# Optimization experiments

Measured on AMD Instinct MI355X. Metric: run time of the kernel, lower is better.

## Reference

```python
import jax, jax.numpy as jnp
import numpy as np

N = 30000      # nodes
IN = 768       # input feature dim
C = 128        # hidden channels (= conv out_dim, = gate dim)
HEADS = 4      # attention heads (TransformerConv and Semantic)
DH = 128       # per-head dim (concat=False -> out_channels)
R = 3          # num relations
E = 80000      # edges per relation
NEG = 0.01     # LeakyReLU slope


def setup_inputs() -> dict:
    key = jax.random.key(0)
    ks = iter(jax.random.split(key, 64))
    def nx(shape):
        return jax.random.normal(next(ks), shape, dtype=jnp.float32) * 0.02
    inp = {}
    inp["x"] = jax.random.normal(next(ks), (N, IN), dtype=jnp.float32)
    inp["edges"] = jax.random.randint(next(ks), (R, 2, E), 0, N, dtype=jnp.int32)
    inp["lin1_W"] = nx((IN, C)); inp["lin1_b"] = jnp.zeros((C,), jnp.float32)
    for l in ("l1", "l2"):
        inp[f"{l}_Wq"] = nx((R, C, HEADS * DH)); inp[f"{l}_bq"] = jnp.zeros((R, HEADS * DH), jnp.float32)
        inp[f"{l}_Wk"] = nx((R, C, HEADS * DH)); inp[f"{l}_bk"] = jnp.zeros((R, HEADS * DH), jnp.float32)
        inp[f"{l}_Wv"] = nx((R, C, HEADS * DH)); inp[f"{l}_bv"] = jnp.zeros((R, HEADS * DH), jnp.float32)
        inp[f"{l}_Ws"] = nx((R, C, DH));         inp[f"{l}_bs"] = jnp.zeros((R, DH), jnp.float32)
        inp[f"{l}_gW"] = nx((C + DH, C));        inp[f"{l}_gb"] = jnp.zeros((C,), jnp.float32)
        inp[f"{l}_sW1"] = nx((HEADS, C, C));     inp[f"{l}_sb1"] = jnp.zeros((HEADS, C), jnp.float32)
        inp[f"{l}_sw2"] = nx((HEADS, C))
    inp["lin2_W"] = nx((C, C)); inp["lin2_b"] = jnp.zeros((C,), jnp.float32)
    inp["clf_W"] = nx((C, 2)); inp["clf_b"] = jnp.zeros((2,), jnp.float32)
    return inp


def lrelu(x):
    return jnp.where(x >= 0, x, NEG * x)


def transformer_conv(x, src, dst, Wq, bq, Wk, bk, Wv, bv, Ws, bs):
    # PyG TransformerConv, heads=HEADS, concat=False (head mean), root_weight=True, eval (no dropout)
    n = x.shape[0]
    q = (x @ Wq + bq).reshape(n, HEADS, DH)
    k = (x @ Wk + bk).reshape(n, HEADS, DH)
    v = (x @ Wv + bv).reshape(n, HEADS, DH)
    logits = (q[dst] * k[src]).sum(-1) / np.sqrt(DH)      # [E, H]
    m = jax.ops.segment_max(logits, dst, num_segments=n)  # scatter-softmax (stable)
    a = jnp.exp(logits - m[dst])
    s = jax.ops.segment_sum(a, dst, num_segments=n)
    alpha = a / s[dst]
    agg = jax.ops.segment_sum(alpha[:, :, None] * v[src], dst, num_segments=n)  # [N, H, DH]
    return agg.mean(axis=1) + x @ Ws + bs


def semantic(Hm, sW1, sb1, sw2):
    # Hm: [N, R, C]; per-head scoring MLP -> softmax over relations -> weighted sum, averaged over heads
    t = jnp.tanh(jnp.einsum('nrc,hco->hnro', Hm, sW1) + sb1[:, None, None, :])  # [H, N, R, C]
    scores = jnp.einsum('hnro,ho->hnr', t, sw2).mean(axis=1)                    # [H, R]
    beta = jax.nn.softmax(scores, axis=-1)
    return jnp.einsum('hr,nrc->nc', beta, Hm) / HEADS


def rgt_layer(x, edges, Wq, bq, Wk, bk, Wv, bv, Ws, bs, gW, gb, sW1, sb1, sw2):
    Hs = []
    for r in range(R):  # small fixed relation loop
        src, dst = edges[r, 0], edges[r, 1]
        U = transformer_conv(x, src, dst, Wq[r], bq[r], Wk[r], bk[r], Wv[r], bv[r], Ws[r], bs[r])
        Z = jax.nn.sigmoid(jnp.concatenate([U, x], axis=1) @ gW + gb)
        Hs.append(jnp.tanh(U) * Z + x * (1.0 - Z))
    Hm = jnp.stack(Hs, axis=1)  # [N, R, C]
    return semantic(Hm, sW1, sb1, sw2)


def reference(x, edges, lin1_W, lin1_b,
              l1_Wq, l1_bq, l1_Wk, l1_bk, l1_Wv, l1_bv, l1_Ws, l1_bs, l1_gW, l1_gb, l1_sW1, l1_sb1, l1_sw2,
              l2_Wq, l2_bq, l2_Wk, l2_bk, l2_Wv, l2_bv, l2_Ws, l2_bs, l2_gW, l2_gb, l2_sW1, l2_sb1, l2_sw2,
              lin2_W, lin2_b, clf_W, clf_b):
    h = lrelu(x @ lin1_W + lin1_b)
    h = rgt_layer(h, edges, l1_Wq, l1_bq, l1_Wk, l1_bk, l1_Wv, l1_bv, l1_Ws, l1_bs, l1_gW, l1_gb, l1_sW1, l1_sb1, l1_sw2)
    h = rgt_layer(h, edges, l2_Wq, l2_bq, l2_Wk, l2_bk, l2_Wv, l2_bv, l2_Ws, l2_bs, l2_gW, l2_gb, l2_sW1, l2_sb1, l2_sw2)
    h = lrelu(h @ lin2_W + lin2_b)
    return h @ clf_W + clf_b
```

## Files before the change

kernel.cpp:

```cpp
#include <hip/hip_runtime.h>
#include <math.h>

#define Nn 30000
#define RR 3
#define EE 80000
#define MT_M 235

#define SAP 72
#define EP_LD 68
#define KBIG 0x40000000

typedef __attribute__((ext_vector_type(8))) short bf16x8;
typedef __attribute__((ext_vector_type(4))) float f32x4;

__device__ __forceinline__ unsigned short f2bf(float f) {
    union { float f; unsigned u; } v; v.f = f;
    unsigned r = v.u + 0x7fff + ((v.u >> 16) & 1);
    return (unsigned short)(r >> 16);
}
__device__ __forceinline__ float bf2f(short h) {
    union { unsigned u; float f; } v;
    v.u = ((unsigned)(unsigned short)h) << 16;
    return v.f;
}
__device__ __forceinline__ float fast_tanh(float x) {
    float e = __expf(2.f * x);
    return 1.f - 2.f / (e + 1.f);
}
__device__ __forceinline__ void unpack8(uint4 u, float* f) {
    union { unsigned u; float f; } a;
    a.u = u.x << 16;          f[0] = a.f;
    a.u = u.x & 0xffff0000u;  f[1] = a.f;
    a.u = u.y << 16;          f[2] = a.f;
    a.u = u.y & 0xffff0000u;  f[3] = a.f;
    a.u = u.z << 16;          f[4] = a.f;
    a.u = u.z & 0xffff0000u;  f[5] = a.f;
    a.u = u.w << 16;          f[6] = a.f;
    a.u = u.w & 0xffff0000u;  f[7] = a.f;
}

__device__ __forceinline__ void mfma_core(
    const short* __restrict__ A, int lda,
    const short* __restrict__ A2, int lda2, int ksplit,
    const short* __restrict__ Bt,
    int M, int K, int m0, int n0,
    short* As, short* Bs, f32x4 (&acc)[4][4])
{
    const int t = threadIdx.x;
    const int srow = t >> 3;
    const int scol = (t & 7) << 3;
    const int lane = t & 63;
    const int wave = t >> 6;
    const int wm = (wave >> 1) << 6;
    const int wn = (wave & 1) << 6;
    const int fr = lane & 15;
    const int quad = lane >> 4;

    for (int k0 = 0; k0 < K; k0 += 64) {
        const short* Abase; int kk0, ldax;
        if (k0 < ksplit) { Abase = A;  kk0 = k0;          ldax = lda;  }
        else             { Abase = A2; kk0 = k0 - ksplit; ldax = lda2; }
        #pragma unroll
        for (int rr = 0; rr < 4; rr++) {
            int r = srow + rr * 32;
            int gr = m0 + r;
            bf16x8 va = {0, 0, 0, 0, 0, 0, 0, 0};
            if (gr < M) va = *(const bf16x8*)(Abase + (size_t)gr * ldax + kk0 + scol);
            *(bf16x8*)(As + r * SAP + scol) = va;
        }
        #pragma unroll
        for (int rr = 0; rr < 4; rr++) {
            int r = srow + rr * 32;
            bf16x8 vb = *(const bf16x8*)(Bt + (size_t)(n0 + r) * K + k0 + scol);
            *(bf16x8*)(Bs + r * SAP + scol) = vb;
        }
        __syncthreads();
        #pragma unroll
        for (int kc = 0; kc < 2; kc++) {
            bf16x8 af[4], bfr[4];
            #pragma unroll
            for (int i = 0; i < 4; i++)
                af[i] = *(const bf16x8*)(As + (wm + i * 16 + fr) * SAP + kc * 32 + quad * 8);
            #pragma unroll
            for (int i = 0; i < 4; i++)
                bfr[i] = *(const bf16x8*)(Bs + (wn + i * 16 + fr) * SAP + kc * 32 + quad * 8);
            #pragma unroll
            for (int mi = 0; mi < 4; mi++)
                #pragma unroll
                for (int ni = 0; ni < 4; ni++)
                    acc[mi][ni] = __builtin_amdgcn_mfma_f32_16x16x32_bf16(
                        af[mi], bfr[ni], acc[mi][ni], 0, 0, 0);
        }
        __syncthreads();
    }
}

__global__ __launch_bounds__(256) void gemm_mfma(
    const short* __restrict__ A, int lda,
    const short* __restrict__ A2, int lda2, int ksplit,
    const short* __restrict__ Bt, const float* __restrict__ bias,
    float* __restrict__ C, int ldc, short* __restrict__ Cbf, int ldcbf,
    int M, int K, int act)
{
    __shared__ short As[128 * SAP];
    __shared__ short Bs[128 * SAP];
    f32x4 acc[4][4];
    #pragma unroll
    for (int i = 0; i < 4; i++)
        #pragma unroll
        for (int j = 0; j < 4; j++) acc[i][j] = (f32x4){0.f, 0.f, 0.f, 0.f};
    int m0 = blockIdx.y * 128, n0 = blockIdx.x * 128;
    mfma_core(A, lda, A2, lda2, ksplit, Bt, M, K, m0, n0, As, Bs, acc);

    const int t = threadIdx.x;
    const int lane = t & 63, wave = t >> 6;
    const int wm = (wave >> 1) << 6, wn = (wave & 1) << 6;
    const int fr = lane & 15, quad = lane >> 4;
    float* ws = (float*)As + wave * 16 * EP_LD;
    const int rrow = lane >> 2;
    const int cseg = (lane & 3) << 4;
    #pragma unroll
    for (int mi = 0; mi < 4; mi++) {
        #pragma unroll
        for (int ni = 0; ni < 4; ni++)
            #pragma unroll
            for (int reg = 0; reg < 4; reg++)
                ws[(quad * 4 + reg) * EP_LD + ni * 16 + fr] = acc[mi][ni][reg];
        int gr = m0 + wm + mi * 16 + rrow;
        if (gr >= M) continue;
        int gc = n0 + wn + cseg;
        float vals[16];
        #pragma unroll
        for (int j = 0; j < 16; j++) {
            float v = ws[rrow * EP_LD + cseg + j] + bias[gc + j];
            if (act == 1) v = (v >= 0.f) ? v : 0.01f * v;
            vals[j] = v;
        }
        if (C) {
            float* cp = C + (size_t)gr * ldc + gc;
            #pragma unroll
            for (int j4 = 0; j4 < 4; j4++)
                *(float4*)(cp + j4 * 4) = make_float4(vals[j4 * 4], vals[j4 * 4 + 1],
                                                      vals[j4 * 4 + 2], vals[j4 * 4 + 3]);
        }
        if (Cbf) {
            unsigned pk[8];
            #pragma unroll
            for (int j2 = 0; j2 < 8; j2++)
                pk[j2] = ((unsigned)f2bf(vals[2 * j2 + 1]) << 16) | (unsigned)f2bf(vals[2 * j2]);
            unsigned* bp = (unsigned*)(Cbf + (size_t)gr * ldcbf + gc);
            *(uint4*)bp       = make_uint4(pk[0], pk[1], pk[2], pk[3]);
            *(uint4*)(bp + 4) = make_uint4(pk[4], pk[5], pk[6], pk[7]);
        }
    }
}

__global__ __launch_bounds__(256) void gemm_qkvs(
    const short* __restrict__ A,
    const short* __restrict__ Wt, const float* __restrict__ bias,
    short* __restrict__ qkv3, short* __restrict__ Ubf, int M)
{
    __shared__ short As[128 * SAP];
    __shared__ short Bs[128 * SAP];
    f32x4 acc[4][4];
    #pragma unroll
    for (int i = 0; i < 4; i++)
        #pragma unroll
        for (int j = 0; j < 4; j++) acc[i][j] = (f32x4){0.f, 0.f, 0.f, 0.f};
    int m0 = blockIdx.y * 128, bx = blockIdx.x, n0 = bx * 128;
    mfma_core(A, 128, A, 128, KBIG, Wt, M, 128, m0, n0, As, Bs, acc);

    const int t = threadIdx.x;
    const int lane = t & 63, wave = t >> 6;
    const int wm = (wave >> 1) << 6, wn = (wave & 1) << 6;
    const int fr = lane & 15, quad = lane >> 4;
    float* ws = (float*)As + wave * 16 * EP_LD;
    const int rrow = lane >> 2;
    const int cseg = (lane & 3) << 4;
    #pragma unroll
    for (int mi = 0; mi < 4; mi++) {
        #pragma unroll
        for (int ni = 0; ni < 4; ni++)
            #pragma unroll
            for (int reg = 0; reg < 4; reg++)
                ws[(quad * 4 + reg) * EP_LD + ni * 16 + fr] = acc[mi][ni][reg];
        int gr = m0 + wm + mi * 16 + rrow;
        if (gr >= M) continue;
        int lc = wn + cseg;
        float vals[16];
        #pragma unroll
        for (int j = 0; j < 16; j++)
            vals[j] = ws[rrow * EP_LD + cseg + j] + bias[n0 + lc + j];
        unsigned pk[8];
        #pragma unroll
        for (int j2 = 0; j2 < 8; j2++)
            pk[j2] = ((unsigned)f2bf(vals[2 * j2 + 1]) << 16) | (unsigned)f2bf(vals[2 * j2]);
        short* dst;
        if (bx < 36) {
            int r = bx / 12;
            dst = qkv3 + ((size_t)(r * Nn + gr)) * 1536 + (bx - r * 12) * 128 + lc;
        } else {
            dst = Ubf + (size_t)gr * 384 + (bx - 36) * 128 + lc;
        }
        unsigned* bp = (unsigned*)dst;
        *(uint4*)bp       = make_uint4(pk[0], pk[1], pk[2], pk[3]);
        *(uint4*)(bp + 4) = make_uint4(pk[4], pk[5], pk[6], pk[7]);
    }
}

__global__ __launch_bounds__(256) void gate_mfma(
    const short* __restrict__ Ubf,
    const short* __restrict__ Hbf,
    const short* __restrict__ gWt, const float* __restrict__ gb,
    const float* __restrict__ Hf,
    float* __restrict__ Hm, short* __restrict__ HmBf,
    int M)
{
    __shared__ short As[128 * SAP];
    __shared__ short Bs[128 * SAP];
    f32x4 acc[4][4];
    #pragma unroll
    for (int i = 0; i < 4; i++)
        #pragma unroll
        for (int j = 0; j < 4; j++) acc[i][j] = (f32x4){0.f, 0.f, 0.f, 0.f};
    int r = blockIdx.z;
    int m0 = blockIdx.y * 128;
    mfma_core(Ubf + r * 128, 384, Hbf, 128, 128, gWt, M, 256, m0, 0, As, Bs, acc);

    const int t = threadIdx.x;
    const int lane = t & 63, wave = t >> 6;
    const int wm = (wave >> 1) << 6, wn = (wave & 1) << 6;
    const int fr = lane & 15, quad = lane >> 4;
    float* ws = (float*)As + wave * 16 * EP_LD;
    const int rrow = lane >> 2;
    const int cseg = (lane & 3) << 4;
    #pragma unroll
    for (int mi = 0; mi < 4; mi++) {
        #pragma unroll
        for (int ni = 0; ni < 4; ni++)
            #pragma unroll
            for (int reg = 0; reg < 4; reg++)
                ws[(quad * 4 + reg) * EP_LD + ni * 16 + fr] = acc[mi][ni][reg];
        int gr = m0 + wm + mi * 16 + rrow;
        if (gr >= M) continue;
        int gc = wn + cseg;
        const short* up = Ubf + (size_t)gr * 384 + r * 128 + gc;
        const float* hp = Hf + (size_t)gr * 128 + gc;
        float uv[16], hv[16];
        uint4 u0 = *(const uint4*)up;
        uint4 u1 = *(const uint4*)(up + 8);
        unpack8(u0, uv); unpack8(u1, uv + 8);
        #pragma unroll
        for (int j4 = 0; j4 < 4; j4++)
            *(float4*)(hv + j4 * 4) = *(const float4*)(hp + j4 * 4);
        float vals[16];
        #pragma unroll
        for (int j = 0; j < 16; j++) {
            float g = ws[rrow * EP_LD + cseg + j] + gb[gc + j];
            float z = 1.f / (1.f + __expf(-g));
            vals[j] = fast_tanh(uv[j]) * z + hv[j] * (1.f - z);
        }
        float* cp = Hm + (size_t)gr * 384 + r * 128 + gc;
        #pragma unroll
        for (int j4 = 0; j4 < 4; j4++)
            *(float4*)(cp + j4 * 4) = make_float4(vals[j4 * 4], vals[j4 * 4 + 1],
                                                  vals[j4 * 4 + 2], vals[j4 * 4 + 3]);
        unsigned pk[8];
        #pragma unroll
        for (int j2 = 0; j2 < 8; j2++)
            pk[j2] = ((unsigned)f2bf(vals[2 * j2 + 1]) << 16) | (unsigned)f2bf(vals[2 * j2]);
        unsigned* bp = (unsigned*)(HmBf + (size_t)gr * 384 + r * 128 + gc);
        *(uint4*)bp       = make_uint4(pk[0], pk[1], pk[2], pk[3]);
        *(uint4*)(bp + 4) = make_uint4(pk[4], pk[5], pk[6], pk[7]);
    }
}

__global__ __launch_bounds__(256) void semantic_mfma(
    const short* __restrict__ HmBf, const short* __restrict__ sW1t,
    const float* __restrict__ sb1, const float* __restrict__ sw2,
    float* __restrict__ partial, int M)
{
    __shared__ short As[128 * SAP];
    __shared__ short Bs[128 * SAP];
    __shared__ float red4[4];
    f32x4 acc[4][4];
    #pragma unroll
    for (int i = 0; i < 4; i++)
        #pragma unroll
        for (int j = 0; j < 4; j++) acc[i][j] = (f32x4){0.f, 0.f, 0.f, 0.f};
    int head = blockIdx.x, r = blockIdx.z;
    int m0 = blockIdx.y * 128, n0 = head * 128;
    mfma_core(HmBf + r * 128, 384, HmBf + r * 128, 384, KBIG, sW1t, M, 128, m0, n0, As, Bs, acc);
    const int t = threadIdx.x;
    const int lane = t & 63, wave = t >> 6;
    const int wm = (wave >> 1) << 6, wn = (wave & 1) << 6;
    const int fr = lane & 15, quad = lane >> 4;
    float local = 0.f;
    #pragma unroll
    for (int ni = 0; ni < 4; ni++) {
        int gc = n0 + wn + ni * 16 + fr;
        float b = sb1[gc], w2 = sw2[gc];
        #pragma unroll
        for (int mi = 0; mi < 4; mi++) {
            #pragma unroll
            for (int reg = 0; reg < 4; reg++) {
                int gr = m0 + wm + mi * 16 + quad * 4 + reg;
                if (gr >= M) continue;
                local += fast_tanh(acc[mi][ni][reg] + b) * w2;
            }
        }
    }
    #pragma unroll
    for (int off = 1; off < 64; off <<= 1) local += __shfl_xor(local, off);
    if (lane == 0) red4[wave] = local;
    __syncthreads();
    if (t == 0)
        partial[(head * 3 + r) * MT_M + blockIdx.y] = red4[0] + red4[1] + red4[2] + red4[3];
}

__global__ void reduce12_kernel(const float* __restrict__ partial, float* __restrict__ scores)
{
    int z = blockIdx.x;
    int lane = threadIdx.x;
    float s = 0.f;
    for (int i = lane; i < MT_M; i += 64) s += partial[z * MT_M + i];
    #pragma unroll
    for (int off = 1; off < 64; off <<= 1) s += __shfl_xor(s, off);
    if (lane == 0) scores[z] = s;
}

__global__ void compute_w_kernel(const float* __restrict__ scores, float* __restrict__ w, float invN)
{
    if (blockIdx.x == 0 && threadIdx.x == 0) {
        float wr[3] = {0.f, 0.f, 0.f};
        for (int h = 0; h < 4; h++) {
            float s0 = scores[h * 3 + 0] * invN;
            float s1 = scores[h * 3 + 1] * invN;
            float s2 = scores[h * 3 + 2] * invN;
            float mx = fmaxf(s0, fmaxf(s1, s2));
            float e0 = __expf(s0 - mx), e1 = __expf(s1 - mx), e2 = __expf(s2 - mx);
            float inv = 1.f / (e0 + e1 + e2);
            wr[0] += 0.25f * e0 * inv;
            wr[1] += 0.25f * e1 * inv;
            wr[2] += 0.25f * e2 * inv;
        }
        w[0] = wr[0]; w[1] = wr[1]; w[2] = wr[2];
    }
}

__global__ void mix_kernel(const float* __restrict__ Hm, const float* __restrict__ w,
                           float* __restrict__ h, short* __restrict__ hbf, int total4)
{
    int i = blockIdx.x * blockDim.x + threadIdx.x;
    if (i >= total4) return;
    int n = i >> 5, c4 = (i & 31) << 2;
    const float* row = Hm + (size_t)n * 384 + c4;
    float4 a = *(const float4*)row;
    float4 b = *(const float4*)(row + 128);
    float4 c = *(const float4*)(row + 256);
    float w0 = w[0], w1 = w[1], w2 = w[2];
    float4 v = make_float4(w0 * a.x + w1 * b.x + w2 * c.x,
                           w0 * a.y + w1 * b.y + w2 * c.y,
                           w0 * a.z + w1 * b.z + w2 * c.z,
                           w0 * a.w + w1 * b.w + w2 * c.w);
    *(float4*)(h + (size_t)n * 128 + c4) = v;
    unsigned p0 = ((unsigned)f2bf(v.y) << 16) | (unsigned)f2bf(v.x);
    unsigned p1 = ((unsigned)f2bf(v.w) << 16) | (unsigned)f2bf(v.z);
    *(uint2*)(hbf + (size_t)n * 128 + c4) = make_uint2(p0, p1);
}

__global__ void convert_bf16_kernel(const float* __restrict__ src, unsigned* __restrict__ dst, int n_pairs)
{
    int i = blockIdx.x * blockDim.x + threadIdx.x;
    if (i >= n_pairs) return;
    float2 f = ((const float2*)src)[i];
    dst[i] = ((unsigned)f2bf(f.y) << 16) | (unsigned)f2bf(f.x);
}

__global__ void prep_global_kernel(const float* __restrict__ lin1_W, const float* __restrict__ lin2_W,
                                   short* __restrict__ lin1Wt, short* __restrict__ lin2Wt)
{
    int id = blockIdx.x * blockDim.x + threadIdx.x;
    if (id < 98304) {
        int n = id / 768, k = id % 768;
        lin1Wt[id] = (short)f2bf(lin1_W[k * 128 + n]);
    } else if (id < 114688) {
        int r = id - 98304;
        int n = r / 128, k = r % 128;
        lin2Wt[r] = (short)f2bf(lin2_W[k * 128 + n]);
    }
}

__global__ void prep_layer_kernel(
    const float* __restrict__ Wq, const float* __restrict__ Wk, const float* __restrict__ Wv,
    const float* __restrict__ Ws, const float* __restrict__ bq, const float* __restrict__ bk,
    const float* __restrict__ bv, const float* __restrict__ bs,
    const float* __restrict__ gW, const float* __restrict__ sW1,
    short* __restrict__ qkvsWt, short* __restrict__ gWt,
    short* __restrict__ sW1t, float* __restrict__ qkvsB)
{
    const int S0 = 638976;
    const int S1 = S0 + 32768;
    const int S2 = S1 + 65536;
    const int S3 = S2 + 4992;
    int id = blockIdx.x * blockDim.x + threadIdx.x;
    if (id < S0) {
        int n = id / 128, k = id - n * 128;
        float v;
        if (n < 4608) {
            int r = n / 1536, j = n - r * 1536;
            if (j < 512)       v = Wq[(size_t)r * 65536 + k * 512 + j];
            else if (j < 1024) v = Wk[(size_t)r * 65536 + k * 512 + (j - 512)];
            else               v = Wv[(size_t)r * 65536 + k * 512 + (j - 1024)];
        } else {
            int m = n - 4608;
            int r = m / 128, c = m - r * 128;
            v = Ws[(size_t)r * 16384 + k * 128 + c];
        }
        qkvsWt[id] = (short)f2bf(v);
    } else if (id < S1) {
        int q = id - S0;
        int n = q / 256, k = q - n * 256;
        gWt[q] = (short)f2bf(gW[k * 128 + n]);
    } else if (id < S2) {
        int q = id - S1;
        int h = q / 16384, rem = q - h * 16384;
        int n = rem / 128, k = rem - n * 128;
        sW1t[q] = (short)f2bf(sW1[(size_t)h * 16384 + k * 128 + n]);
    } else if (id < S3) {
        int q = id - S2;
        float v;
        if (q < 4608) {
            int r = q / 1536, j = q - r * 1536;
            if (j < 512)       v = bq[r * 512 + j];
            else if (j < 1024) v = bk[r * 512 + (j - 512)];
            else               v = bv[r * 512 + (j - 1024)];
        } else {
            v = bs[q - 4608];
        }
        qkvsB[q] = v;
    }
}

__global__ void zero_i32_kernel(int* __restrict__ p, int n)
{
    int i = blockIdx.x * blockDim.x + threadIdx.x;
    if (i < n) p[i] = 0;
}

__global__ void hist3_kernel(const int* __restrict__ edges, int* __restrict__ cnt3)
{
    int i = blockIdx.x * blockDim.x + threadIdx.x;
    if (i >= 3 * EE) return;
    int r = i / EE, e = i - r * EE;
    int d = edges[(size_t)r * 2 * EE + EE + e];
    atomicAdd(&cnt3[r * Nn + d], 1);
}

__global__ __launch_bounds__(1024) void scan3_kernel(const int* __restrict__ cnt3,
                                                     int* __restrict__ rowptr3)
{
    __shared__ int part[1024];
    const int r = blockIdx.x;
    const int* cnt = cnt3 + r * Nn;
    int* rowptr = rowptr3 + r * (Nn + 1);
    int tid = threadIdx.x;
    int per = (Nn + 1023) >> 10;
    int base = tid * per;
    int s = 0;
    for (int i = 0; i < per; i++) {
        int idx = base + i;
        if (idx < Nn) s += cnt[idx];
    }
    part[tid] = s;
    __syncthreads();
    for (int off = 1; off < 1024; off <<= 1) {
        int val = (tid >= off) ? part[tid - off] : 0;
        __syncthreads();
        part[tid] += val;
        __syncthreads();
    }
    int excl = (tid == 0) ? 0 : part[tid - 1];
    for (int i = 0; i < per; i++) {
        int idx = base + i;
        if (idx < Nn) { rowptr[idx] = excl; excl += cnt[idx]; }
    }
    if (tid == 1023) rowptr[Nn] = part[1023];
}

__global__ void scatter3_kernel(const int* __restrict__ edges,
                                const int* __restrict__ rowptr3, int* __restrict__ fill3,
                                int* __restrict__ col3)
{
    int i = blockIdx.x * blockDim.x + threadIdx.x;
    if (i >= 3 * EE) return;
    int r = i / EE, e = i - r * EE;
    int src = edges[(size_t)r * 2 * EE + e];
    int d   = edges[(size_t)r * 2 * EE + EE + e];
    int pos = rowptr3[r * (Nn + 1) + d] + atomicAdd(&fill3[r * Nn + d], 1);
    col3[r * EE + pos] = src;
}

__global__ __launch_bounds__(256) void attn_kernel(
    const short* __restrict__ qkv3,
    const int* __restrict__ rowptr3, const int* __restrict__ col3,
    short* __restrict__ Ubf)
{
    int wid = ((blockIdx.x * blockDim.x + threadIdx.x) >> 6);
    int lane = threadIdx.x & 63;
    if (wid >= 3 * Nn) return;
    int r = wid / Nn, n = wid - r * Nn;
    const short* qkv = qkv3 + (size_t)r * Nn * 1536;
    const int* rowptr = rowptr3 + r * (Nn + 1);
    const int* colb = col3 + r * EE;
    int beg = rowptr[n], end = rowptr[n + 1];

    uint4 qv = ((const uint4*)(qkv + (size_t)n * 1536))[lane];
    float qf[8];
    unpack8(qv, qf);

    float m = -INFINITY, s = 0.f;
    float acc[8] = {0.f, 0.f, 0.f, 0.f, 0.f, 0.f, 0.f, 0.f};
    const float scale = 0.088388347648318447f;

    for (int i = beg; i < end; i++) {
        int src = colb[i];
        const short* base = qkv + (size_t)src * 1536;
        uint4 kv4 = ((const uint4*)(base + 512))[lane];
        uint4 vv4 = ((const uint4*)(base + 1024))[lane];
        float kf[8];
        unpack8(kv4, kf);
        float p = qf[0] * kf[0] + qf[1] * kf[1] + qf[2] * kf[2] + qf[3] * kf[3]
                + qf[4] * kf[4] + qf[5] * kf[5] + qf[6] * kf[6] + qf[7] * kf[7];
        p += __shfl_xor(p, 1);
        p += __shfl_xor(p, 2);
        p += __shfl_xor(p, 4);
        p += __shfl_xor(p, 8);
        float l = p * scale;
        float nm = fmaxf(m, l);
        float sc = __expf(m - nm);
        float pe = __expf(l - nm);
        float vf[8];
        unpack8(vv4, vf);
        s = s * sc + pe;
        #pragma unroll
        for (int j = 0; j < 8; j++) acc[j] = acc[j] * sc + pe * vf[j];
        m = nm;
    }

    float inv = (s > 0.f) ? 1.f / s : 0.f;
    #pragma unroll
    for (int j = 0; j < 8; j++) acc[j] *= inv;
    #pragma unroll
    for (int j = 0; j < 8; j++) acc[j] += __shfl_xor(acc[j], 16);
    #pragma unroll
    for (int j = 0; j < 8; j++) acc[j] += __shfl_xor(acc[j], 32);

    if (lane < 16) {
        short* urow = Ubf + (size_t)n * 384 + r * 128 + lane * 8;
        uint4 old = *(uint4*)urow;
        float sv[8];
        unpack8(old, sv);
        #pragma unroll
        for (int j = 0; j < 8; j++) sv[j] += 0.25f * acc[j];
        unsigned p0 = ((unsigned)f2bf(sv[1]) << 16) | (unsigned)f2bf(sv[0]);
        unsigned p1 = ((unsigned)f2bf(sv[3]) << 16) | (unsigned)f2bf(sv[2]);
        unsigned p2 = ((unsigned)f2bf(sv[5]) << 16) | (unsigned)f2bf(sv[4]);
        unsigned p3 = ((unsigned)f2bf(sv[7]) << 16) | (unsigned)f2bf(sv[6]);
        *(uint4*)urow = make_uint4(p0, p1, p2, p3);
    }
}

__global__ void clf_kernel(const float* __restrict__ t, const float* __restrict__ W,
                           const float* __restrict__ b, float* __restrict__ out, int M)
{
    int n = blockIdx.x * blockDim.x + threadIdx.x;
    if (n >= M) return;
    const float* row = t + (size_t)n * 128;
    float a0 = b[0], a1 = b[1];
    #pragma unroll
    for (int kk = 0; kk < 128; kk++) {
        float a = row[kk];
        a0 += a * W[kk * 2];
        a1 += a * W[kk * 2 + 1];
    }
    out[n * 2] = a0;
    out[n * 2 + 1] = a1;
}

extern "C" void kernel_launch(void* const* d_in, const int* in_sizes, int n_in,
                              void* d_out, int out_size, void* d_ws, size_t ws_size,
                              hipStream_t stream)
{
    const float* x      = (const float*)d_in[0];
    const int*   edges  = (const int*)d_in[1];
    const float* lin1_W = (const float*)d_in[2];
    const float* lin1_b = (const float*)d_in[3];
    const int L0 = 4, L1 = 17;
    const float* lin2_W = (const float*)d_in[30];
    const float* lin2_b = (const float*)d_in[31];
    const float* clf_W  = (const float*)d_in[32];
    const float* clf_b  = (const float*)d_in[33];
    float* out = (float*)d_out;

    char* w = (char*)d_ws;
    size_t off = 0;
    auto alloc = [&](size_t bytes) { void* p = w + off; off = (off + bytes + 255) & ~(size_t)255; return p; };
    float* h      = (float*)alloc((size_t)Nn * 128 * 4);
    short* h_bf   = (short*)alloc((size_t)Nn * 128 * 2);
    short* U_bf   = (short*)alloc((size_t)Nn * 384 * 2);
    char* BIG     = (char*)alloc((size_t)3 * Nn * 1536 * 2);
    short* qkv3   = (short*)BIG;
    short* x_bf   = (short*)BIG;
    float* Hm     = (float*)BIG;
    short* Hm_bf  = (short*)(BIG + (size_t)Nn * 384 * 4);
    float* lin2o  = (float*)BIG;
    short* lin1Wt = (short*)alloc((size_t)98304 * 2);
    short* lin2Wt = (short*)alloc((size_t)16384 * 2);
    short* qkvsWt = (short*)alloc((size_t)2 * 638976 * 2);
    short* gWt    = (short*)alloc((size_t)2 * 32768 * 2);
    short* sW1t   = (short*)alloc((size_t)2 * 65536 * 2);
    float* qkvsB  = (float*)alloc((size_t)2 * 4992 * 4);
    int* rowptr3  = (int*)alloc((size_t)3 * (Nn + 1) * 4);
    int* cnt3     = (int*)alloc((size_t)3 * Nn * 4);
    int* col3     = (int*)alloc((size_t)3 * EE * 4);
    float* partial = (float*)alloc((size_t)12 * MT_M * 4);
    float* scores = (float*)alloc(12 * 4);
    float* wmix   = (float*)alloc(3 * 4);

    const int MT = MT_M;
    dim3 blk(256);

    {
        int n_pairs = Nn * 768 / 2;
        convert_bf16_kernel<<<(n_pairs + 255) / 256, blk, 0, stream>>>(x, (unsigned*)x_bf, n_pairs);
        prep_global_kernel<<<(114688 + 255) / 256, blk, 0, stream>>>(lin1_W, lin2_W, lin1Wt, lin2Wt);
        for (int l = 0; l < 2; l++) {
            int base = (l == 0) ? L0 : L1;
            prep_layer_kernel<<<(742272 + 255) / 256, blk, 0, stream>>>(
                (const float*)d_in[base + 0], (const float*)d_in[base + 2], (const float*)d_in[base + 4],
                (const float*)d_in[base + 6], (const float*)d_in[base + 1], (const float*)d_in[base + 3],
                (const float*)d_in[base + 5], (const float*)d_in[base + 7],
                (const float*)d_in[base + 8], (const float*)d_in[base + 10],
                qkvsWt + (size_t)l * 638976, gWt + (size_t)l * 32768,
                sW1t + (size_t)l * 65536, qkvsB + (size_t)l * 4992);
        }
        zero_i32_kernel<<<(3 * Nn + 255) / 256, blk, 0, stream>>>(cnt3, 3 * Nn);
        hist3_kernel<<<(3 * EE + 255) / 256, blk, 0, stream>>>(edges, cnt3);
        scan3_kernel<<<3, 1024, 0, stream>>>(cnt3, rowptr3);
        zero_i32_kernel<<<(3 * Nn + 255) / 256, blk, 0, stream>>>(cnt3, 3 * Nn);
        scatter3_kernel<<<(3 * EE + 255) / 256, blk, 0, stream>>>(edges, rowptr3, cnt3, col3);
    }

    gemm_mfma<<<dim3(1, MT), blk, 0, stream>>>(
        x_bf, 768, x_bf, 768, KBIG, lin1Wt, lin1_b, h, 128, h_bf, 128, Nn, 768, 1);

    for (int l = 0; l < 2; l++) {
        int base = (l == 0) ? L0 : L1;
        const float* gb  = (const float*)d_in[base + 9];
        const float* sb1 = (const float*)d_in[base + 11];
        const float* sw2 = (const float*)d_in[base + 12];
        short* lqkvsWt = qkvsWt + (size_t)l * 638976;
        short* lgWt    = gWt + (size_t)l * 32768;
        short* lsW1t   = sW1t + (size_t)l * 65536;
        float* lqkvsB  = qkvsB + (size_t)l * 4992;

        gemm_qkvs<<<dim3(39, MT), blk, 0, stream>>>(
            h_bf, lqkvsWt, lqkvsB, qkv3, U_bf, Nn);

        attn_kernel<<<(3 * Nn + 3) / 4, blk, 0, stream>>>(qkv3, rowptr3, col3, U_bf);

        gate_mfma<<<dim3(1, MT, 3), blk, 0, stream>>>(
            U_bf, h_bf, lgWt, gb, h, Hm, Hm_bf, Nn);

        semantic_mfma<<<dim3(4, MT, 3), blk, 0, stream>>>(Hm_bf, lsW1t, sb1, sw2, partial, Nn);
        reduce12_kernel<<<12, 64, 0, stream>>>(partial, scores);
        compute_w_kernel<<<1, 64, 0, stream>>>(scores, wmix, 1.f / (float)Nn);
        mix_kernel<<<(Nn * 32 + 255) / 256, blk, 0, stream>>>(Hm, wmix, h, h_bf, Nn * 32);
    }

    gemm_mfma<<<dim3(1, MT), blk, 0, stream>>>(
        h_bf, 128, h_bf, 128, KBIG, lin2Wt, lin2_b, lin2o, 128, (short*)nullptr, 0, Nn, 128, 1);
    clf_kernel<<<(Nn + 255) / 256, blk, 0, stream>>>(lin2o, clf_W, clf_b, out, Nn);
}
```

Before: 980.8 us.

## Fuse gate and semantic GEMMs, convert x to bf16 inside lin1 GEMM

Merges the gate GEMM epilogue with the semantic-attention GEMM. The gated Hm tile is kept as bf16 in shared memory and multiplied against each head's sW1 slice in the same block, which removes the Hm_bf global round trip and one launch. The lin1 GEMM now reads fp32 x directly and converts it to bf16 while staging tiles, dropping the separate conversion pass. The two score-reduction kernels are merged into one. The cost is more shared memory per block (lower occupancy) and serial per-head loops inside gate_sem.

Result: no change. 984.9 us (+0.4%).

```diff
diff --git a/kernel.cpp b/kernel.cpp
--- a/kernel.cpp
+++ b/kernel.cpp
@@ -7,7 +7,8 @@
 #define MT_M 235
 
 #define SAP 72
-#define EP_LD 68
+#define SAP2 136
+#define EP_LD 70
 #define KBIG 0x40000000
 
 typedef __attribute__((ext_vector_type(8))) short bf16x8;
@@ -17,11 +18,6 @@
     union { float f; unsigned u; } v; v.f = f;
     unsigned r = v.u + 0x7fff + ((v.u >> 16) & 1);
     return (unsigned short)(r >> 16);
-}
-__device__ __forceinline__ float bf2f(short h) {
-    union { unsigned u; float f; } v;
-    v.u = ((unsigned)(unsigned short)h) << 16;
-    return v.f;
 }
 __device__ __forceinline__ float fast_tanh(float x) {
     float e = __expf(2.f * x);
@@ -155,6 +151,109 @@
     }
 }
 
+__global__ __launch_bounds__(256) void gemm_lin1(
+    const float* __restrict__ A, int lda,
+    const short* __restrict__ Bt, const float* __restrict__ bias,
+    float* __restrict__ C, int ldc, short* __restrict__ Cbf, int ldcbf,
+    int M, int K, int act)
+{
+    __shared__ short As[128 * SAP];
+    __shared__ short Bs[128 * SAP];
+    f32x4 acc[4][4];
+    #pragma unroll
+    for (int i = 0; i < 4; i++)
+        #pragma unroll
+        for (int j = 0; j < 4; j++) acc[i][j] = (f32x4){0.f, 0.f, 0.f, 0.f};
+    int m0 = blockIdx.y * 128, n0 = blockIdx.x * 128;
+
+    const int t = threadIdx.x;
+    const int srow = t >> 3;
+    const int scol = (t & 7) << 3;
+    const int lane = t & 63;
+    const int wave = t >> 6;
+    const int wm = (wave >> 1) << 6;
+    const int wn = (wave & 1) << 6;
+    const int fr = lane & 15;
+    const int quad = lane >> 4;
+
+    for (int k0 = 0; k0 < K; k0 += 64) {
+        #pragma unroll
+        for (int rr = 0; rr < 4; rr++) {
+            int r = srow + rr * 32;
+            int gr = m0 + r;
+            unsigned pk[4] = {0, 0, 0, 0};
+            if (gr < M) {
+                const float* ap = A + (size_t)gr * lda + k0 + scol;
+                float4 f0 = *(const float4*)ap;
+                float4 f1 = *(const float4*)(ap + 4);
+                pk[0] = ((unsigned)f2bf(f0.y) << 16) | (unsigned)f2bf(f0.x);
+                pk[1] = ((unsigned)f2bf(f0.w) << 16) | (unsigned)f2bf(f0.z);
+                pk[2] = ((unsigned)f2bf(f1.y) << 16) | (unsigned)f2bf(f1.x);
+                pk[3] = ((unsigned)f2bf(f1.w) << 16) | (unsigned)f2bf(f1.z);
+            }
+            *(uint4*)(As + r * SAP + scol) = make_uint4(pk[0], pk[1], pk[2], pk[3]);
+        }
+        #pragma unroll
+        for (int rr = 0; rr < 4; rr++) {
+            int r = srow + rr * 32;
+            bf16x8 vb = *(const bf16x8*)(Bt + (size_t)(n0 + r) * K + k0 + scol);
+            *(bf16x8*)(Bs + r * SAP + scol) = vb;
+        }
+        __syncthreads();
+        #pragma unroll
+        for (int kc = 0; kc < 2; kc++) {
+            bf16x8 af[4], bfr[4];
+            #pragma unroll
+            for (int i = 0; i < 4; i++)
+                af[i] = *(const bf16x8*)(As + (wm + i * 16 + fr) * SAP + kc * 32 + quad * 8);
+            #pragma unroll
+            for (int i = 0; i < 4; i++)
+                bfr[i] = *(const bf16x8*)(Bs + (wn + i * 16 + fr) * SAP + kc * 32 + quad * 8);
+            #pragma unroll
+            for (int mi = 0; mi < 4; mi++)
+                #pragma unroll
+                for (int ni = 0; ni < 4; ni++)
+                    acc[mi][ni] = __builtin_amdgcn_mfma_f32_16x16x32_bf16(
+                        af[mi], bfr[ni], acc[mi][ni], 0, 0, 0);
+        }
+        __syncthreads();
+    }
+
+    float* ws = (float*)As + wave * 16 * EP_LD;
+    const int rrow = lane >> 2;
+    const int cseg = (lane & 3) << 4;
+    #pragma unroll
+    for (int mi = 0; mi < 4; mi++) {
+        #pragma unroll
+        for (int ni = 0; ni < 4; ni++)
+            #pragma unroll
+            for (int reg = 0; reg < 4; reg++)
+                ws[(quad * 4 + reg) * EP_LD + ni * 16 + fr] = acc[mi][ni][reg];
+        int gr = m0 + wm + mi * 16 + rrow;
+        if (gr >= M) continue;
+        int gc = n0 + wn + cseg;
+        float vals[16];
+        #pragma unroll
+        for (int j = 0; j < 16; j++) {
+            float v = ws[rrow * EP_LD + cseg + j] + bias[gc + j];
+            if (act == 1) v = (v >= 0.f) ? v : 0.01f * v;
+            vals[j] = v;
+        }
+        float* cp = C + (size_t)gr * ldc + gc;
+        #pragma unroll
+        for (int j4 = 0; j4 < 4; j4++)
+            *(float4*)(cp + j4 * 4) = make_float4(vals[j4 * 4], vals[j4 * 4 + 1],
+                                                  vals[j4 * 4 + 2], vals[j4 * 4 + 3]);
+        unsigned pk[8];
+        #pragma unroll
+        for (int j2 = 0; j2 < 8; j2++)
+            pk[j2] = ((unsigned)f2bf(vals[2 * j2 + 1]) << 16) | (unsigned)f2bf(vals[2 * j2]);
+        unsigned* bp = (unsigned*)(Cbf + (size_t)gr * ldcbf + gc);
+        *(uint4*)bp       = make_uint4(pk[0], pk[1], pk[2], pk[3]);
+        *(uint4*)(bp + 4) = make_uint4(pk[4], pk[5], pk[6], pk[7]);
+    }
+}
+
 __global__ __launch_bounds__(256) void gemm_qkvs(
     const short* __restrict__ A,
     const short* __restrict__ Wt, const float* __restrict__ bias,
@@ -208,16 +307,22 @@
     }
 }
 
-__global__ __launch_bounds__(256) void gate_mfma(
+__global__ __launch_bounds__(256) void gate_sem(
     const short* __restrict__ Ubf,
     const short* __restrict__ Hbf,
     const short* __restrict__ gWt, const float* __restrict__ gb,
     const float* __restrict__ Hf,
-    float* __restrict__ Hm, short* __restrict__ HmBf,
-    int M)
-{
-    __shared__ short As[128 * SAP];
-    __shared__ short Bs[128 * SAP];
+    const short* __restrict__ sW1t,
+    const float* __restrict__ sb1, const float* __restrict__ sw2,
+    float* __restrict__ Hm,
+    float* __restrict__ partial, int M)
+{
+    __shared__ short L0[128 * 144];
+    __shared__ short HmT[128 * SAP2];
+    __shared__ float redL[16];
+    short* As = L0;
+    short* Bs = L0 + 128 * SAP;
+
     f32x4 acc[4][4];
     #pragma unroll
     for (int i = 0; i < 4; i++)
@@ -228,12 +333,15 @@
     mfma_core(Ubf + r * 128, 384, Hbf, 128, 128, gWt, M, 256, m0, 0, As, Bs, acc);
 
     const int t = threadIdx.x;
+    const int srow = t >> 3;
+    const int scol = (t & 7) << 3;
     const int lane = t & 63, wave = t >> 6;
     const int wm = (wave >> 1) << 6, wn = (wave & 1) << 6;
     const int fr = lane & 15, quad = lane >> 4;
     float* ws = (float*)As + wave * 16 * EP_LD;
     const int rrow = lane >> 2;
     const int cseg = (lane & 3) << 4;
+
     #pragma unroll
     for (int mi = 0; mi < 4; mi++) {
         #pragma unroll
@@ -241,102 +349,118 @@
             #pragma unroll
             for (int reg = 0; reg < 4; reg++)
                 ws[(quad * 4 + reg) * EP_LD + ni * 16 + fr] = acc[mi][ni][reg];
-        int gr = m0 + wm + mi * 16 + rrow;
-        if (gr >= M) continue;
+        int row = wm + mi * 16 + rrow;
+        int gr = m0 + row;
         int gc = wn + cseg;
-        const short* up = Ubf + (size_t)gr * 384 + r * 128 + gc;
-        const float* hp = Hf + (size_t)gr * 128 + gc;
-        float uv[16], hv[16];
-        uint4 u0 = *(const uint4*)up;
-        uint4 u1 = *(const uint4*)(up + 8);
-        unpack8(u0, uv); unpack8(u1, uv + 8);
-        #pragma unroll
-        for (int j4 = 0; j4 < 4; j4++)
-            *(float4*)(hv + j4 * 4) = *(const float4*)(hp + j4 * 4);
-        float vals[16];
-        #pragma unroll
-        for (int j = 0; j < 16; j++) {
-            float g = ws[rrow * EP_LD + cseg + j] + gb[gc + j];
-            float z = 1.f / (1.f + __expf(-g));
-            vals[j] = fast_tanh(uv[j]) * z + hv[j] * (1.f - z);
-        }
-        float* cp = Hm + (size_t)gr * 384 + r * 128 + gc;
-        #pragma unroll
-        for (int j4 = 0; j4 < 4; j4++)
-            *(float4*)(cp + j4 * 4) = make_float4(vals[j4 * 4], vals[j4 * 4 + 1],
-                                                  vals[j4 * 4 + 2], vals[j4 * 4 + 3]);
-        unsigned pk[8];
-        #pragma unroll
-        for (int j2 = 0; j2 < 8; j2++)
-            pk[j2] = ((unsigned)f2bf(vals[2 * j2 + 1]) << 16) | (unsigned)f2bf(vals[2 * j2]);
-        unsigned* bp = (unsigned*)(HmBf + (size_t)gr * 384 + r * 128 + gc);
-        *(uint4*)bp       = make_uint4(pk[0], pk[1], pk[2], pk[3]);
-        *(uint4*)(bp + 4) = make_uint4(pk[4], pk[5], pk[6], pk[7]);
-    }
-}
-
-__global__ __launch_bounds__(256) void semantic_mfma(
-    const short* __restrict__ HmBf, const short* __restrict__ sW1t,
-    const float* __restrict__ sb1, const float* __restrict__ sw2,
-    float* __restrict__ partial, int M)
-{
-    __shared__ short As[128 * SAP];
-    __shared__ short Bs[128 * SAP];
-    __shared__ float red4[4];
-    f32x4 acc[4][4];
-    #pragma unroll
-    for (int i = 0; i < 4; i++)
-        #pragma unroll
-        for (int j = 0; j < 4; j++) acc[i][j] = (f32x4){0.f, 0.f, 0.f, 0.f};
-    int head = blockIdx.x, r = blockIdx.z;
-    int m0 = blockIdx.y * 128, n0 = head * 128;
-    mfma_core(HmBf + r * 128, 384, HmBf + r * 128, 384, KBIG, sW1t, M, 128, m0, n0, As, Bs, acc);
-    const int t = threadIdx.x;
-    const int lane = t & 63, wave = t >> 6;
-    const int wm = (wave >> 1) << 6, wn = (wave & 1) << 6;
-    const int fr = lane & 15, quad = lane >> 4;
-    float local = 0.f;
-    #pragma unroll
-    for (int ni = 0; ni < 4; ni++) {
-        int gc = n0 + wn + ni * 16 + fr;
-        float b = sb1[gc], w2 = sw2[gc];
-        #pragma unroll
-        for (int mi = 0; mi < 4; mi++) {
-            #pragma unroll
-            for (int reg = 0; reg < 4; reg++) {
-                int gr = m0 + wm + mi * 16 + quad * 4 + reg;
-                if (gr >= M) continue;
-                local += fast_tanh(acc[mi][ni][reg] + b) * w2;
+        unsigned pk[8] = {0, 0, 0, 0, 0, 0, 0, 0};
+        if (gr < M) {
+            const short* up = Ubf + (size_t)gr * 384 + r * 128 + gc;
+            const float* hp = Hf + (size_t)gr * 128 + gc;
+            float uv[16], hv[16];
+            uint4 u0 = *(const uint4*)up;
+            uint4 u1 = *(const uint4*)(up + 8);
+            unpack8(u0, uv); unpack8(u1, uv + 8);
+            #pragma unroll
+            for (int j4 = 0; j4 < 4; j4++)
+                *(float4*)(hv + j4 * 4) = *(const float4*)(hp + j4 * 4);
+            float vals[16];
+            #pragma unroll
+            for (int j = 0; j < 16; j++) {
+                float g = ws[rrow * EP_LD + cseg + j] + gb[gc + j];
+                float z = 1.f / (1.f + __expf(-g));
+                vals[j] = fast_tanh(uv[j]) * z + hv[j] * (1.f - z);
             }
-        }
-    }
-    #pragma unroll
-    for (int off = 1; off < 64; off <<= 1) local += __shfl_xor(local, off);
-    if (lane == 0) red4[wave] = local;
+            float* cp = Hm + (size_t)gr * 384 + r * 128 + gc;
+            #pragma unroll
+            for (int j4 = 0; j4 < 4; j4++)
+                *(float4*)(cp + j4 * 4) = make_float4(vals[j4 * 4], vals[j4 * 4 + 1],
+                                                      vals[j4 * 4 + 2], vals[j4 * 4 + 3]);
+            #pragma unroll
+            for (int j2 = 0; j2 < 8; j2++)
+                pk[j2] = ((unsigned)f2bf(vals[2 * j2 + 1]) << 16) | (unsigned)f2bf(vals[2 * j2]);
+        }
+        unsigned* hp2 = (unsigned*)(HmT + row * SAP2 + gc);
+        *(uint4*)hp2       = make_uint4(pk[0], pk[1], pk[2], pk[3]);
+        *(uint4*)(hp2 + 4) = make_uint4(pk[4], pk[5], pk[6], pk[7]);
+    }
+
+    for (int h = 0; h < 4; h++) {
+        __syncthreads();
+        const short* Bh = sW1t + (size_t)h * 128 * 128;
+        #pragma unroll
+        for (int rr2 = 0; rr2 < 4; rr2++) {
+            int n = srow + rr2 * 32;
+            #pragma unroll
+            for (int half = 0; half < 2; half++) {
+                bf16x8 vb = *(const bf16x8*)(Bh + n * 128 + half * 64 + scol);
+                *(bf16x8*)(L0 + n * SAP2 + half * 64 + scol) = vb;
+            }
+        }
+        __syncthreads();
+        f32x4 acc2[4][4];
+        #pragma unroll
+        for (int i = 0; i < 4; i++)
+            #pragma unroll
+            for (int j = 0; j < 4; j++) acc2[i][j] = (f32x4){0.f, 0.f, 0.f, 0.f};
+        #pragma unroll
+        for (int kc = 0; kc < 4; kc++) {
+            bf16x8 af[4], bfr[4];
+            #pragma unroll
+            for (int i = 0; i < 4; i++)
+                af[i] = *(const bf16x8*)(HmT + (wm + i * 16 + fr) * SAP2 + kc * 32 + quad * 8);
+            #pragma unroll
+            for (int i = 0; i < 4; i++)
+                bfr[i] = *(const bf16x8*)(L0 + (wn + i * 16 + fr) * SAP2 + kc * 32 + quad * 8);
+            #pragma unroll
+            for (int mi = 0; mi < 4; mi++)
+                #pragma unroll
+                for (int ni = 0; ni < 4; ni++)
+                    acc2[mi][ni] = __builtin_amdgcn_mfma_f32_16x16x32_bf16(
+                        af[mi], bfr[ni], acc2[mi][ni], 0, 0, 0);
+        }
+        float local = 0.f;
+        #pragma unroll
+        for (int ni = 0; ni < 4; ni++) {
+            int gcl = h * 128 + wn + ni * 16 + fr;
+            float b = sb1[gcl], w2 = sw2[gcl];
+            #pragma unroll
+            for (int mi = 0; mi < 4; mi++) {
+                #pragma unroll
+                for (int reg = 0; reg < 4; reg++) {
+                    int gr = m0 + wm + mi * 16 + quad * 4 + reg;
+                    if (gr < M) local += fast_tanh(acc2[mi][ni][reg] + b) * w2;
+                }
+            }
+        }
+        #pragma unroll
+        for (int off = 1; off < 64; off <<= 1) local += __shfl_xor(local, off);
+        if (lane == 0) redL[h * 4 + wave] = local;
+    }
     __syncthreads();
-    if (t == 0)
-        partial[(head * 3 + r) * MT_M + blockIdx.y] = red4[0] + red4[1] + red4[2] + red4[3];
-}
-
-__global__ void reduce12_kernel(const float* __restrict__ partial, float* __restrict__ scores)
-{
-    int z = blockIdx.x;
-    int lane = threadIdx.x;
-    float s = 0.f;
-    for (int i = lane; i < MT_M; i += 64) s += partial[z * MT_M + i];
-    #pragma unroll
-    for (int off = 1; off < 64; off <<= 1) s += __shfl_xor(s, off);
-    if (lane == 0) scores[z] = s;
-}
-
-__global__ void compute_w_kernel(const float* __restrict__ scores, float* __restrict__ w, float invN)
-{
-    if (blockIdx.x == 0 && threadIdx.x == 0) {
+    if (t < 4) {
+        float s = redL[t * 4] + redL[t * 4 + 1] + redL[t * 4 + 2] + redL[t * 4 + 3];
+        partial[(t * 3 + r) * MT_M + blockIdx.y] = s;
+    }
+}
+
+__global__ void compute_w2(const float* __restrict__ partial, float* __restrict__ w, float invN)
+{
+    int t = threadIdx.x;
+    float sz[12];
+    #pragma unroll
+    for (int z = 0; z < 12; z++) {
+        float s = 0.f;
+        for (int i = t; i < MT_M; i += 64) s += partial[z * MT_M + i];
+        #pragma unroll
+        for (int off = 1; off < 64; off <<= 1) s += __shfl_xor(s, off);
+        sz[z] = s;
+    }
+    if (t == 0) {
         float wr[3] = {0.f, 0.f, 0.f};
         for (int h = 0; h < 4; h++) {
-            float s0 = scores[h * 3 + 0] * invN;
-            float s1 = scores[h * 3 + 1] * invN;
-            float s2 = scores[h * 3 + 2] * invN;
+            float s0 = sz[h * 3 + 0] * invN;
+            float s1 = sz[h * 3 + 1] * invN;
+            float s2 = sz[h * 3 + 2] * invN;
             float mx = fmaxf(s0, fmaxf(s1, s2));
             float e0 = __expf(s0 - mx), e1 = __expf(s1 - mx), e2 = __expf(s2 - mx);
             float inv = 1.f / (e0 + e1 + e2);
@@ -367,14 +491,6 @@
     unsigned p0 = ((unsigned)f2bf(v.y) << 16) | (unsigned)f2bf(v.x);
     unsigned p1 = ((unsigned)f2bf(v.w) << 16) | (unsigned)f2bf(v.z);
     *(uint2*)(hbf + (size_t)n * 128 + c4) = make_uint2(p0, p1);
-}
-
-__global__ void convert_bf16_kernel(const float* __restrict__ src, unsigned* __restrict__ dst, int n_pairs)
-{
-    int i = blockIdx.x * blockDim.x + threadIdx.x;
-    if (i >= n_pairs) return;
-    float2 f = ((const float2*)src)[i];
-    dst[i] = ((unsigned)f2bf(f.y) << 16) | (unsigned)f2bf(f.x);
 }
 
 __global__ void prep_global_kernel(const float* __restrict__ lin1_W, const float* __restrict__ lin2_W,
@@ -611,9 +727,7 @@
     short* U_bf   = (short*)alloc((size_t)Nn * 384 * 2);
     char* BIG     = (char*)alloc((size_t)3 * Nn * 1536 * 2);
     short* qkv3   = (short*)BIG;
-    short* x_bf   = (short*)BIG;
     float* Hm     = (float*)BIG;
-    short* Hm_bf  = (short*)(BIG + (size_t)Nn * 384 * 4);
     float* lin2o  = (float*)BIG;
     short* lin1Wt = (short*)alloc((size_t)98304 * 2);
     short* lin2Wt = (short*)alloc((size_t)16384 * 2);
@@ -625,15 +739,12 @@
     int* cnt3     = (int*)alloc((size_t)3 * Nn * 4);
     int* col3     = (int*)alloc((size_t)3 * EE * 4);
     float* partial = (float*)alloc((size_t)12 * MT_M * 4);
-    float* scores = (float*)alloc(12 * 4);
     float* wmix   = (float*)alloc(3 * 4);
 
     const int MT = MT_M;
     dim3 blk(256);
 
     {
-        int n_pairs = Nn * 768 / 2;
-        convert_bf16_kernel<<<(n_pairs + 255) / 256, blk, 0, stream>>>(x, (unsigned*)x_bf, n_pairs);
         prep_global_kernel<<<(114688 + 255) / 256, blk, 0, stream>>>(lin1_W, lin2_W, lin1Wt, lin2Wt);
         for (int l = 0; l < 2; l++) {
             int base = (l == 0) ? L0 : L1;
@@ -652,8 +763,8 @@
         scatter3_kernel<<<(3 * EE + 255) / 256, blk, 0, stream>>>(edges, rowptr3, cnt3, col3);
     }
 
-    gemm_mfma<<<dim3(1, MT), blk, 0, stream>>>(
-        x_bf, 768, x_bf, 768, KBIG, lin1Wt, lin1_b, h, 128, h_bf, 128, Nn, 768, 1);
+    gemm_lin1<<<dim3(1, MT), blk, 0, stream>>>(
+        x, 768, lin1Wt, lin1_b, h, 128, h_bf, 128, Nn, 768, 1);
 
     for (int l = 0; l < 2; l++) {
         int base = (l == 0) ? L0 : L1;
@@ -670,12 +781,10 @@
 
         attn_kernel<<<(3 * Nn + 3) / 4, blk, 0, stream>>>(qkv3, rowptr3, col3, U_bf);
 
-        gate_mfma<<<dim3(1, MT, 3), blk, 0, stream>>>(
-            U_bf, h_bf, lgWt, gb, h, Hm, Hm_bf, Nn);
-
-        semantic_mfma<<<dim3(4, MT, 3), blk, 0, stream>>>(Hm_bf, lsW1t, sb1, sw2, partial, Nn);
-        reduce12_kernel<<<12, 64, 0, stream>>>(partial, scores);
-        compute_w_kernel<<<1, 64, 0, stream>>>(scores, wmix, 1.f / (float)Nn);
+        gate_sem<<<dim3(1, MT, 3), blk, 0, stream>>>(
+            U_bf, h_bf, lgWt, gb, h, lsW1t, sb1, sw2, Hm, partial, Nn);
+
+        compute_w2<<<1, 64, 0, stream>>>(partial, wmix, 1.f / (float)Nn);
         mix_kernel<<<(Nn * 32 + 255) / 256, blk, 0, stream>>>(Hm, wmix, h, h_bf, Nn * 32);
     }
 
```
